# Kernel optimization log

Hardware: AMD Instinct MI355X
Metric: run time of the kernel (lower is better)

The kernel has to match this reference:

```python
import jax, jax.numpy as jnp
import numpy as np

N = 4096                 # num nodes
SP, GE, TE = 256, 8, 64  # modality input dims
E = 32                   # embed_dim == hidden_features == out_features
H = 2                    # num_heads
D3 = 3 * E               # combined dim = 96
NEG_SLOPE = 0.2


def setup_inputs() -> dict:
    key = jax.random.key(0)
    ks = iter(jax.random.split(key, 64))
    nrm = lambda shape, s=0.05: jax.random.normal(next(ks), shape, jnp.float32) * s
    inp = {
        "spatial": jax.random.normal(next(ks), (N, SP), jnp.float32),
        "genomic": jax.random.normal(next(ks), (N, GE), jnp.float32),
        "temporal": jax.random.normal(next(ks), (N, TE), jnp.float32),
        "adj_matrix": jax.random.randint(next(ks), (N, N), 0, 2, jnp.int32),
        # modality embedding MLPs (Linear + LayerNorm)
        "sp_w": nrm((SP, E)), "sp_b": jnp.zeros((E,)), "sp_lg": jnp.ones((E,)), "sp_lb": jnp.zeros((E,)),
        "ge_w": nrm((GE, E)), "ge_b": jnp.zeros((E,)), "ge_lg": jnp.ones((E,)), "ge_lb": jnp.zeros((E,)),
        "te_w": nrm((TE, E)), "te_b": jnp.zeros((E,)), "te_lg": jnp.ones((E,)), "te_lb": jnp.zeros((E,)),
        # GAT: W_shared [96 -> H*E], attention vector a [2E], out_proj [H*E -> E], LayerNorm(E)
        "gat_w": nrm((D3, H * E)), "gat_a": nrm((2 * E,)),
        "gat_ow": nrm((H * E, E)), "gat_ob": jnp.zeros((E,)),
        "gat_lg": jnp.ones((E,)), "gat_lb": jnp.zeros((E,)),
        # MultiheadAttention (embed 96): packed qkv in_proj and out_proj
        "mha_iw": nrm((D3, 3 * D3)), "mha_ib": jnp.zeros((3 * D3,)),
        "mha_ow": nrm((D3, D3)), "mha_ob": jnp.zeros((D3,)),
        # motor tower
        "m1_w": nrm((D3, 2 * E)), "m1_b": jnp.zeros((2 * E,)), "m1_lg": jnp.ones((2 * E,)), "m1_lb": jnp.zeros((2 * E,)),
        "m2_w": nrm((2 * E, E)), "m2_b": jnp.zeros((E,)), "m2_lg": jnp.ones((E,)), "m2_lb": jnp.zeros((E,)),
        "m3_w": nrm((E, 1)), "m3_b": jnp.zeros((1,)),
        # cognitive tower
        "c1_w": nrm((D3, 2 * E)), "c1_b": jnp.zeros((2 * E,)), "c1_lg": jnp.ones((2 * E,)), "c1_lb": jnp.zeros((2 * E,)),
        "c2_w": nrm((2 * E, E)), "c2_b": jnp.zeros((E,)), "c2_lg": jnp.ones((E,)), "c2_lb": jnp.zeros((E,)),
        "c3_w": nrm((E, 1)), "c3_b": jnp.zeros((1,)),
    }
    return inp


def _ln(x, g, b, eps=1e-5):
    m = x.mean(-1, keepdims=True)
    v = ((x - m) ** 2).mean(-1, keepdims=True)
    return (x - m) / jnp.sqrt(v + eps) * g + b


def _embed(x, w, b, lg, lb):
    return jax.nn.relu(_ln(x @ w + b, lg, lb))  # dropout is identity in eval


def _tower(x, w1, b1, lg1, lb1, w2, b2, lg2, lb2, w3, b3):
    h = jax.nn.relu(_ln(x @ w1 + b1, lg1, lb1))
    h = jax.nn.relu(_ln(h @ w2 + b2, lg2, lb2))
    return h @ w3 + b3


def reference(spatial, genomic, temporal, adj_matrix,
              sp_w, sp_b, sp_lg, sp_lb, ge_w, ge_b, ge_lg, ge_lb,
              te_w, te_b, te_lg, te_lb,
              gat_w, gat_a, gat_ow, gat_ob, gat_lg, gat_lb,
              mha_iw, mha_ib, mha_ow, mha_ob,
              m1_w, m1_b, m1_lg, m1_lb, m2_w, m2_b, m2_lg, m2_lb, m3_w, m3_b,
              c1_w, c1_b, c1_lg, c1_lb, c2_w, c2_b, c2_lg, c2_lb, c3_w, c3_b):
    n = spatial.shape[0]
    s_emb = _embed(spatial, sp_w, sp_b, sp_lg, sp_lb)
    g_emb = _embed(genomic, ge_w, ge_b, ge_lg, ge_lb)
    t_emb = _embed(temporal, te_w, te_b, te_lg, te_lb)
    combined = jnp.concatenate([s_emb, g_emb, t_emb], axis=-1)  # [N, 96]

    # --- TaskSpecificGAT ---
    h = (combined @ gat_w).reshape(n, H, E)  # [N, H, E]
    # e[i,j] = leaky_relu(a . [h_i ; h_j]) = leaky_relu((h @ a1)_i + (h @ a2)_j)
    a1, a2 = gat_a[:E], gat_a[E:]
    f1 = jnp.einsum('nhd,d->nh', h, a1)  # source term
    f2 = jnp.einsum('nhd,d->nh', h, a2)  # target term
    e = jax.nn.leaky_relu(f1[:, None, :] + f2[None, :, :], NEG_SLOPE)  # [N, N, H]
    e = jnp.where(adj_matrix[:, :, None] == 0, -jnp.inf, e)
    alpha = jax.nn.softmax(e, axis=1)  # softmax over neighbors j
    h_out = jnp.einsum('ijh,jhd->ihd', alpha, h).reshape(n, H * E)  # [N, 64]
    gat_out = _ln(h_out @ gat_ow + gat_ob, gat_lg, gat_lb)  # [N, 32]

    # gat_expanded = cat([gat_out]*3) -> [N, 96], attn over seq_len=1
    gx = jnp.tile(gat_out, (1, 3))
    # MHA with a single key/query: softmax over one key == 1, so output = out_proj(v)
    v = gx @ mha_iw[:, 2 * D3:] + mha_ib[2 * D3:]
    attn_out = v @ mha_ow + mha_ob

    final = attn_out + combined
    motor = _tower(final, m1_w, m1_b, m1_lg, m1_lb, m2_w, m2_b, m2_lg, m2_lb, m3_w, m3_b)
    cognitive = jax.nn.sigmoid(
        _tower(final, c1_w, c1_b, c1_lg, c1_lb, c2_w, c2_b, c2_lg, c2_lb, c3_w, c3_b))
    return (motor, cognitive)
```

## Files before the change

kernel.cpp:

```cpp
#include <hip/hip_runtime.h>
#include <math.h>

#define NN 4096
#define LOG2E 1.4426950408889634f

typedef short short8 __attribute__((ext_vector_type(8)));
typedef float f32x4 __attribute__((ext_vector_type(4)));

#define OFF_COMB   0u
#define OFF_F1     393216u
#define OFF_F2     401408u
#define OFF_MAXF2  409600u
#define OFF_W2     409616u
#define OFF_B2     412688u
#define OFF_HT     412800u
#define OFF_PART   543872u

__device__ inline unsigned short f2bf(float x) {
  unsigned u = __float_as_uint(x);
  unsigned r = u + 0x7FFFu + ((u >> 16) & 1u);
  return (unsigned short)(r >> 16);
}

__global__ __launch_bounds__(256) void k_comb(
    const float* __restrict__ spatial, const float* __restrict__ genomic,
    const float* __restrict__ temporal,
    const float* __restrict__ sp_w, const float* __restrict__ sp_b,
    const float* __restrict__ sp_lg, const float* __restrict__ sp_lb,
    const float* __restrict__ ge_w, const float* __restrict__ ge_b,
    const float* __restrict__ ge_lg, const float* __restrict__ ge_lb,
    const float* __restrict__ te_w, const float* __restrict__ te_b,
    const float* __restrict__ te_lg, const float* __restrict__ te_lb,
    const float* __restrict__ mha_iw, const float* __restrict__ mha_ib,
    const float* __restrict__ mha_ow, const float* __restrict__ mha_ob,
    float* __restrict__ ws)
{
  int t = threadIdx.x;
  int blk = blockIdx.x;

  if (blk >= 1536) {
    if (blk < 1548) {
      int idx = (blk - 1536) * 256 + t;
      int b = idx / 96, col = idx - b * 96;
      float acc = 0.f;
      for (int r = 0; r < 96; r++) {
        float fw = mha_iw[b * 288 + 192 + r]
                 + mha_iw[(b + 32) * 288 + 192 + r]
                 + mha_iw[(b + 64) * 288 + 192 + r];
        acc = fmaf(fw, mha_ow[r * 96 + col], acc);
      }
      ws[OFF_W2 + b * 96 + col] = acc;
    } else {
      if (t < 96) {
        float acc = mha_ob[t];
        for (int r = 0; r < 96; r++) acc = fmaf(mha_ib[192 + r], mha_ow[r * 96 + t], acc);
        ws[OFF_B2 + t] = acc;
      }
    }
    return;
  }

  int j = blk * 8 + (t >> 5);
  int grp = j >> 12;
  int row = j & 4095;
  int c = t & 31;

  float val;
  const float* lg;
  const float* lb;
  if (grp == 0) {
    const float* in = spatial + (size_t)row * 256;
    float a0 = 0.f, a1 = 0.f, a2 = 0.f, a3 = 0.f;
#pragma unroll 4
    for (int k = 0; k < 256; k += 4) {
      float4 x = *(const float4*)(in + k);
      a0 = fmaf(x.x, sp_w[(k)     * 32 + c], a0);
      a1 = fmaf(x.y, sp_w[(k + 1) * 32 + c], a1);
      a2 = fmaf(x.z, sp_w[(k + 2) * 32 + c], a2);
      a3 = fmaf(x.w, sp_w[(k + 3) * 32 + c], a3);
    }
    val = sp_b[c] + ((a0 + a1) + (a2 + a3));
    lg = sp_lg; lb = sp_lb;
  } else if (grp == 1) {
    const float* in = genomic + (size_t)row * 8;
    float4 x0 = *(const float4*)(in);
    float4 x1 = *(const float4*)(in + 4);
    float a0 = ge_b[c];
    a0 = fmaf(x0.x, ge_w[0 * 32 + c], a0);
    a0 = fmaf(x0.y, ge_w[1 * 32 + c], a0);
    a0 = fmaf(x0.z, ge_w[2 * 32 + c], a0);
    a0 = fmaf(x0.w, ge_w[3 * 32 + c], a0);
    a0 = fmaf(x1.x, ge_w[4 * 32 + c], a0);
    a0 = fmaf(x1.y, ge_w[5 * 32 + c], a0);
    a0 = fmaf(x1.z, ge_w[6 * 32 + c], a0);
    a0 = fmaf(x1.w, ge_w[7 * 32 + c], a0);
    val = a0;
    lg = ge_lg; lb = ge_lb;
  } else {
    const float* in = temporal + (size_t)row * 64;
    float a0 = 0.f, a1 = 0.f, a2 = 0.f, a3 = 0.f;
#pragma unroll 4
    for (int k = 0; k < 64; k += 4) {
      float4 x = *(const float4*)(in + k);
      a0 = fmaf(x.x, te_w[(k)     * 32 + c], a0);
      a1 = fmaf(x.y, te_w[(k + 1) * 32 + c], a1);
      a2 = fmaf(x.z, te_w[(k + 2) * 32 + c], a2);
      a3 = fmaf(x.w, te_w[(k + 3) * 32 + c], a3);
    }
    val = te_b[c] + ((a0 + a1) + (a2 + a3));
    lg = te_lg; lb = te_lb;
  }

  float s1 = val, s2 = val * val;
#pragma unroll
  for (int m = 1; m < 32; m <<= 1) {
    s1 += __shfl_xor(s1, m, 32);
    s2 += __shfl_xor(s2, m, 32);
  }
  float mean = s1 * (1.f / 32.f);
  float var  = s2 * (1.f / 32.f) - mean * mean;
  float y = fmaxf((val - mean) * rsqrtf(var + 1e-5f) * lg[c] + lb[c], 0.f);
  ws[OFF_COMB + (size_t)row * 96 + grp * 32 + c] = y;
}

__global__ __launch_bounds__(256) void k_proj(
    const float* __restrict__ gat_w, const float* __restrict__ gat_a,
    float* __restrict__ ws)
{
  __shared__ float h_s[4][64];
  int t = threadIdx.x;
  int w = t >> 6, d = t & 63;
  int row0 = blockIdx.x * 4;
  int row = row0 + w;

  const float* crow = ws + OFF_COMB + (size_t)row * 96;
  float a0 = 0.f, a1 = 0.f;
#pragma unroll 8
  for (int k = 0; k < 96; k += 2) {
    a0 = fmaf(crow[k],     gat_w[k * 64 + d],       a0);
    a1 = fmaf(crow[k + 1], gat_w[(k + 1) * 64 + d], a1);
  }
  float h = a0 + a1;

  int dc = d & 31;
  float p1 = h * gat_a[dc];
  float p2 = h * gat_a[32 + dc];
#pragma unroll
  for (int m = 1; m < 32; m <<= 1) {
    p1 += __shfl_xor(p1, m, 32);
    p2 += __shfl_xor(p2, m, 32);
  }
  if (dc == 0) {
    int head = d >> 5;
    ws[OFF_F1 + head * NN + row] = p1;
    ws[OFF_F2 + head * NN + row] = p2;
  }

  h_s[w][d] = h;
  __syncthreads();
  if (t < 64) {
    unsigned u0 = (unsigned)f2bf(h_s[0][t]) | ((unsigned)f2bf(h_s[1][t]) << 16);
    unsigned u1 = (unsigned)f2bf(h_s[2][t]) | ((unsigned)f2bf(h_s[3][t]) << 16);
    uint2 v; v.x = u0; v.y = u1;
    unsigned short* hT = (unsigned short*)(ws + OFF_HT);
    *(uint2*)(hT + (size_t)t * NN + row0) = v;
  }
}

__global__ __launch_bounds__(256) void k_max(float* __restrict__ ws)
{
  __shared__ float red[4][2];
  int t = threadIdx.x;
  const float4* p0 = (const float4*)(ws + OFF_F2);
  const float4* p1 = (const float4*)(ws + OFF_F2 + NN);
  float m0 = -1e30f, m1 = -1e30f;
#pragma unroll
  for (int q = 0; q < 4; q++) {
    float4 v0 = p0[t + q * 256];
    float4 v1 = p1[t + q * 256];
    m0 = fmaxf(m0, fmaxf(fmaxf(v0.x, v0.y), fmaxf(v0.z, v0.w)));
    m1 = fmaxf(m1, fmaxf(fmaxf(v1.x, v1.y), fmaxf(v1.z, v1.w)));
  }
#pragma unroll
  for (int m = 1; m < 64; m <<= 1) {
    m0 = fmaxf(m0, __shfl_xor(m0, m));
    m1 = fmaxf(m1, __shfl_xor(m1, m));
  }
  if ((t & 63) == 0) { red[t >> 6][0] = m0; red[t >> 6][1] = m1; }
  __syncthreads();
  if (t == 0) {
    float r0 = red[0][0], r1 = red[0][1];
    for (int q = 1; q < 4; q++) { r0 = fmaxf(r0, red[q][0]); r1 = fmaxf(r1, red[q][1]); }
    ws[OFF_MAXF2] = r0;
    ws[OFF_MAXF2 + 1] = r1;
  }
}

__global__ __launch_bounds__(256) void k_gat3(
    const int* __restrict__ adj,
    const unsigned short* __restrict__ hT,
    const float* __restrict__ f1h,
    const float* __restrict__ f2h,
    const float* __restrict__ maxf2,
    float* __restrict__ part,
    float* __restrict__ lpart, int NS)
{
  int t = threadIdx.x;
  int lane = t & 63, wv = t >> 6;
  int quad = lane >> 4, mrow = lane & 15;
  int ib = blockIdx.x * 64 + wv * 16;
  int i_lane = ib + mrow;
  int slice = NN / NS;
  int jb = blockIdx.y * slice;

  float f1v0 = f1h[i_lane];
  float f1v1 = f1h[NN + i_lane];
  float s0 = f1v0 + maxf2[0], s1 = f1v1 + maxf2[1];
  float sh0 = fmaxf(s0, 0.2f * s0);
  float sh1 = fmaxf(s1, 0.2f * s1);
  float c00 = -sh0 * LOG2E;
  float c01 = -sh1 * LOG2E;

  f32x4 acc00 = {0.f, 0.f, 0.f, 0.f};
  f32x4 acc01 = {0.f, 0.f, 0.f, 0.f};
  f32x4 acc10 = {0.f, 0.f, 0.f, 0.f};
  f32x4 acc11 = {0.f, 0.f, 0.f, 0.f};
  float ls0 = 0.f, ls1 = 0.f;

  const int* adjRow = adj + (size_t)i_lane * NN;

#pragma unroll 2
  for (int jc = jb; jc < jb + slice; jc += 32) {
    int jq = jc + quad * 8;
    int4 am0 = *(const int4*)(adjRow + jq);
    int4 am1 = *(const int4*)(adjRow + jq + 4);
    float4 fa = *(const float4*)(f2h + jq);
    float4 fb = *(const float4*)(f2h + jq + 4);
    float4 fc = *(const float4*)(f2h + NN + jq);
    float4 fd = *(const float4*)(f2h + NN + jq + 4);
    short8 b00 = *(const short8*)(hT + (size_t)(mrow)      * NN + jq);
    short8 b01 = *(const short8*)(hT + (size_t)(16 + mrow) * NN + jq);
    short8 b10 = *(const short8*)(hT + (size_t)(32 + mrow) * NN + jq);
    short8 b11 = *(const short8*)(hT + (size_t)(48 + mrow) * NN + jq);

    float f2a[8] = {fa.x, fa.y, fa.z, fa.w, fb.x, fb.y, fb.z, fb.w};
    float f2b[8] = {fc.x, fc.y, fc.z, fc.w, fd.x, fd.y, fd.z, fd.w};
    int   amv[8] = {am0.x, am0.y, am0.z, am0.w, am1.x, am1.y, am1.z, am1.w};

    union { short8 v; unsigned short u[8]; } a0, a1;
#pragma unroll
    for (int k = 0; k < 8; k++) {
      float e0 = f1v0 + f2a[k];
      float le0 = fmaxf(e0, 0.2f * e0);
      float w0 = __builtin_amdgcn_exp2f(fmaf(le0, LOG2E, c00));
      float e1 = f1v1 + f2b[k];
      float le1 = fmaxf(e1, 0.2f * e1);
      float w1 = __builtin_amdgcn_exp2f(fmaf(le1, LOG2E, c01));
      w0 = amv[k] ? w0 : 0.f;
      w1 = amv[k] ? w1 : 0.f;
      ls0 += w0; ls1 += w1;
      a0.u[k] = f2bf(w0);
      a1.u[k] = f2bf(w1);
    }
    acc00 = __builtin_amdgcn_mfma_f32_16x16x32_bf16(a0.v, b00, acc00, 0, 0, 0);
    acc01 = __builtin_amdgcn_mfma_f32_16x16x32_bf16(a0.v, b01, acc01, 0, 0, 0);
    acc10 = __builtin_amdgcn_mfma_f32_16x16x32_bf16(a1.v, b10, acc10, 0, 0, 0);
    acc11 = __builtin_amdgcn_mfma_f32_16x16x32_bf16(a1.v, b11, acc11, 0, 0, 0);
  }

  ls0 += __shfl_xor(ls0, 16); ls0 += __shfl_xor(ls0, 32);
  ls1 += __shfl_xor(ls1, 16); ls1 += __shfl_xor(ls1, 32);

  int slot = blockIdx.y;
#pragma unroll
  for (int r = 0; r < 4; r++) {
    int ig = ib + quad * 4 + r;
    float* p = part + (size_t)ig * (NS * 64) + slot * 64;
    p[mrow]      = acc00[r];
    p[16 + mrow] = acc01[r];
    p[32 + mrow] = acc10[r];
    p[48 + mrow] = acc11[r];
  }
  if (lane < 16) {
    int ig = ib + lane;
    lpart[((size_t)ig * NS + slot) * 2]     = ls0;
    lpart[((size_t)ig * NS + slot) * 2 + 1] = ls1;
  }
}

__global__ __launch_bounds__(256) void k_post2(
    const float* __restrict__ gat_ow, const float* __restrict__ gat_ob,
    const float* __restrict__ gat_lg, const float* __restrict__ gat_lb,
    const float* __restrict__ m1_w, const float* __restrict__ m1_b,
    const float* __restrict__ m1_lg, const float* __restrict__ m1_lb,
    const float* __restrict__ m2_w, const float* __restrict__ m2_b,
    const float* __restrict__ m2_lg, const float* __restrict__ m2_lb,
    const float* __restrict__ m3_w, const float* __restrict__ m3_b,
    const float* __restrict__ c1_w, const float* __restrict__ c1_b,
    const float* __restrict__ c1_lg, const float* __restrict__ c1_lb,
    const float* __restrict__ c2_w, const float* __restrict__ c2_b,
    const float* __restrict__ c2_lg, const float* __restrict__ c2_lb,
    const float* __restrict__ c3_w, const float* __restrict__ c3_b,
    const float* __restrict__ part, const float* __restrict__ lpart,
    const float* __restrict__ comb, const float* __restrict__ W2,
    const float* __restrict__ B2,
    float* __restrict__ out, int NS)
{
  int t = threadIdx.x;
  int w = t >> 6, l = t & 63;
  int i = blockIdx.x * 4 + w;

  __shared__ float sh_h[4][64];
  __shared__ float sh_go[4][32];
  __shared__ float sh_fin[4][96];
  __shared__ float sh_t1[4][2][64];

  {
    const float* pr = part + (size_t)i * (NS * 64);
    float a0 = 0.f, a1 = 0.f, a2 = 0.f, a3 = 0.f;
#pragma unroll
    for (int s = 0; s < 16; s += 4) {
      a0 += pr[(s)     * 64 + l];
      a1 += pr[(s + 1) * 64 + l];
      a2 += pr[(s + 2) * 64 + l];
      a3 += pr[(s + 3) * 64 + l];
    }
    float a = (a0 + a1) + (a2 + a3);
    const float* lr = lpart + (size_t)i * NS * 2;
    float l0 = 0.f, l1 = 0.f;
#pragma unroll
    for (int s = 0; s < 16; s++) { l0 += lr[s * 2]; l1 += lr[s * 2 + 1]; }
    sh_h[w][l] = a / (l < 32 ? l0 : l1);
  }
  __syncthreads();

  if (l < 32) {
    float acc = gat_ob[l];
#pragma unroll 8
    for (int r = 0; r < 64; r++) acc = fmaf(sh_h[w][r], gat_ow[r * 32 + l], acc);
    float s1 = acc, s2 = acc * acc;
#pragma unroll
    for (int m = 1; m < 32; m <<= 1) {
      s1 += __shfl_xor(s1, m, 32);
      s2 += __shfl_xor(s2, m, 32);
    }
    float mean = s1 * (1.f / 32.f), var = s2 * (1.f / 32.f) - mean * mean;
    sh_go[w][l] = (acc - mean) * rsqrtf(var + 1e-5f) * gat_lg[l] + gat_lb[l];
  }
  __syncthreads();

  {
    float accA = B2[l];
#pragma unroll 8
    for (int d = 0; d < 32; d++) accA = fmaf(sh_go[w][d], W2[d * 96 + l], accA);
    sh_fin[w][l] = accA + comb[(size_t)i * 96 + l];
    if (l < 32) {
      float accB = B2[64 + l];
#pragma unroll 8
      for (int d = 0; d < 32; d++) accB = fmaf(sh_go[w][d], W2[d * 96 + 64 + l], accB);
      sh_fin[w][64 + l] = accB + comb[(size_t)i * 96 + 64 + l];
    }
  }
  __syncthreads();

  {
    float am = m1_b[l], ac = c1_b[l];
#pragma unroll 4
    for (int r = 0; r < 96; r++) {
      float f = sh_fin[w][r];
      am = fmaf(f, m1_w[r * 64 + l], am);
      ac = fmaf(f, c1_w[r * 64 + l], ac);
    }
    float s1 = am, s2 = am * am;
#pragma unroll
    for (int m = 1; m < 64; m <<= 1) { s1 += __shfl_xor(s1, m); s2 += __shfl_xor(s2, m); }
    float mean = s1 * (1.f / 64.f), var = s2 * (1.f / 64.f) - mean * mean;
    sh_t1[w][0][l] = fmaxf((am - mean) * rsqrtf(var + 1e-5f) * m1_lg[l] + m1_lb[l], 0.f);
    s1 = ac; s2 = ac * ac;
#pragma unroll
    for (int m = 1; m < 64; m <<= 1) { s1 += __shfl_xor(s1, m); s2 += __shfl_xor(s2, m); }
    mean = s1 * (1.f / 64.f); var = s2 * (1.f / 64.f) - mean * mean;
    sh_t1[w][1][l] = fmaxf((ac - mean) * rsqrtf(var + 1e-5f) * c1_lg[l] + c1_lb[l], 0.f);
  }
  __syncthreads();

  {
    int tw = l >> 5, c = l & 31;
    const float* w2  = tw ? c2_w  : m2_w;
    const float* b2  = tw ? c2_b  : m2_b;
    const float* lg2 = tw ? c2_lg : m2_lg;
    const float* lb2 = tw ? c2_lb : m2_lb;
    float a2 = b2[c];
#pragma unroll 4
    for (int r = 0; r < 64; r++) a2 = fmaf(sh_t1[w][tw][r], w2[r * 32 + c], a2);
    float u1 = a2, u2 = a2 * a2;
#pragma unroll
    for (int m = 1; m < 32; m <<= 1) {
      u1 += __shfl_xor(u1, m, 32);
      u2 += __shfl_xor(u2, m, 32);
    }
    float mean = u1 * (1.f / 32.f), var = u2 * (1.f / 32.f) - mean * mean;
    float y2 = fmaxf((a2 - mean) * rsqrtf(var + 1e-5f) * lg2[c] + lb2[c], 0.f);
    float p = y2 * (tw ? c3_w[c] : m3_w[c]);
#pragma unroll
    for (int m = 1; m < 32; m <<= 1) p += __shfl_xor(p, m, 32);
    if (c == 0) {
      float v = p + (tw ? c3_b[0] : m3_b[0]);
      if (tw) out[NN + i] = 1.f / (1.f + expf(-v));
      else    out[i] = v;
    }
  }
}

extern "C" void kernel_launch(void* const* d_in, const int* in_sizes, int n_in,
                              void* d_out, int out_size, void* d_ws, size_t ws_size,
                              hipStream_t stream) {
  (void)in_sizes; (void)n_in; (void)out_size;
  const float* spatial  = (const float*)d_in[0];
  const float* genomic  = (const float*)d_in[1];
  const float* temporal = (const float*)d_in[2];
  const int*   adj      = (const int*)d_in[3];
  const float* sp_w = (const float*)d_in[4];
  const float* sp_b = (const float*)d_in[5];
  const float* sp_lg = (const float*)d_in[6];
  const float* sp_lb = (const float*)d_in[7];
  const float* ge_w = (const float*)d_in[8];
  const float* ge_b = (const float*)d_in[9];
  const float* ge_lg = (const float*)d_in[10];
  const float* ge_lb = (const float*)d_in[11];
  const float* te_w = (const float*)d_in[12];
  const float* te_b = (const float*)d_in[13];
  const float* te_lg = (const float*)d_in[14];
  const float* te_lb = (const float*)d_in[15];
  const float* gat_w = (const float*)d_in[16];
  const float* gat_a = (const float*)d_in[17];
  const float* gat_ow = (const float*)d_in[18];
  const float* gat_ob = (const float*)d_in[19];
  const float* gat_lg = (const float*)d_in[20];
  const float* gat_lb = (const float*)d_in[21];
  const float* mha_iw = (const float*)d_in[22];
  const float* mha_ib = (const float*)d_in[23];
  const float* mha_ow = (const float*)d_in[24];
  const float* mha_ob = (const float*)d_in[25];
  const float* m1_w = (const float*)d_in[26];
  const float* m1_b = (const float*)d_in[27];
  const float* m1_lg = (const float*)d_in[28];
  const float* m1_lb = (const float*)d_in[29];
  const float* m2_w = (const float*)d_in[30];
  const float* m2_b = (const float*)d_in[31];
  const float* m2_lg = (const float*)d_in[32];
  const float* m2_lb = (const float*)d_in[33];
  const float* m3_w = (const float*)d_in[34];
  const float* m3_b = (const float*)d_in[35];
  const float* c1_w = (const float*)d_in[36];
  const float* c1_b = (const float*)d_in[37];
  const float* c1_lg = (const float*)d_in[38];
  const float* c1_lb = (const float*)d_in[39];
  const float* c2_w = (const float*)d_in[40];
  const float* c2_b = (const float*)d_in[41];
  const float* c2_lg = (const float*)d_in[42];
  const float* c2_lb = (const float*)d_in[43];
  const float* c3_w = (const float*)d_in[44];
  const float* c3_b = (const float*)d_in[45];

  float* ws  = (float*)d_ws;
  float* out = (float*)d_out;

  int NS = 16;
  while (NS > 1) {
    size_t need = (size_t)(OFF_PART + (size_t)NS * NN * 64 + (size_t)NS * NN * 2) * 4;
    if (need <= ws_size) break;
    NS >>= 1;
  }
  float* part  = ws + OFF_PART;
  float* lpart = part + (size_t)NS * NN * 64;

  k_comb<<<1549, 256, 0, stream>>>(spatial, genomic, temporal,
                                   sp_w, sp_b, sp_lg, sp_lb,
                                   ge_w, ge_b, ge_lg, ge_lb,
                                   te_w, te_b, te_lg, te_lb,
                                   mha_iw, mha_ib, mha_ow, mha_ob, ws);
  k_proj<<<NN / 4, 256, 0, stream>>>(gat_w, gat_a, ws);
  k_max<<<1, 256, 0, stream>>>(ws);
  dim3 g2(NN / 64, NS);
  k_gat3<<<g2, 256, 0, stream>>>(adj,
                                 (const unsigned short*)(ws + OFF_HT),
                                 ws + OFF_F1, ws + OFF_F2, ws + OFF_MAXF2,
                                 part, lpart, NS);
  k_post2<<<NN / 4, 256, 0, stream>>>(gat_ow, gat_ob, gat_lg, gat_lb,
                                      m1_w, m1_b, m1_lg, m1_lb,
                                      m2_w, m2_b, m2_lg, m2_lb,
                                      m3_w, m3_b,
                                      c1_w, c1_b, c1_lg, c1_lb,
                                      c2_w, c2_b, c2_lg, c2_lb,
                                      c3_w, c3_b,
                                      part, lpart, ws + OFF_COMB,
                                      ws + OFF_W2, ws + OFF_B2,
                                      out, NS);
}
```

Before: 260.3 us.

## Drop max-shift kernel, template GAT split count and raise j-split to 32

Removes the separate f2 max-reduction kernel and the softmax max shift, so exp is computed on the raw leaky-relu score; this saves one launch and a few ops per element but risks overflow or bf16 range issues if scores grow large. The GAT aggregation and post kernels are templated on the split count, so the inner loop fully unrolls. When workspace allows, the neighbour dimension is split 32 ways instead of 16 for more blocks. The cost is more partial sums to write and reduce.

```diff
diff --git a/kernel.cpp b/kernel.cpp
--- a/kernel.cpp
+++ b/kernel.cpp
@@ -10,7 +10,6 @@
 #define OFF_COMB   0u
 #define OFF_F1     393216u
 #define OFF_F2     401408u
-#define OFF_MAXF2  409600u
 #define OFF_W2     409616u
 #define OFF_B2     412688u
 #define OFF_HT     412800u
@@ -167,59 +166,25 @@
   }
 }
 
-__global__ __launch_bounds__(256) void k_max(float* __restrict__ ws)
-{
-  __shared__ float red[4][2];
-  int t = threadIdx.x;
-  const float4* p0 = (const float4*)(ws + OFF_F2);
-  const float4* p1 = (const float4*)(ws + OFF_F2 + NN);
-  float m0 = -1e30f, m1 = -1e30f;
-#pragma unroll
-  for (int q = 0; q < 4; q++) {
-    float4 v0 = p0[t + q * 256];
-    float4 v1 = p1[t + q * 256];
-    m0 = fmaxf(m0, fmaxf(fmaxf(v0.x, v0.y), fmaxf(v0.z, v0.w)));
-    m1 = fmaxf(m1, fmaxf(fmaxf(v1.x, v1.y), fmaxf(v1.z, v1.w)));
-  }
-#pragma unroll
-  for (int m = 1; m < 64; m <<= 1) {
-    m0 = fmaxf(m0, __shfl_xor(m0, m));
-    m1 = fmaxf(m1, __shfl_xor(m1, m));
-  }
-  if ((t & 63) == 0) { red[t >> 6][0] = m0; red[t >> 6][1] = m1; }
-  __syncthreads();
-  if (t == 0) {
-    float r0 = red[0][0], r1 = red[0][1];
-    for (int q = 1; q < 4; q++) { r0 = fmaxf(r0, red[q][0]); r1 = fmaxf(r1, red[q][1]); }
-    ws[OFF_MAXF2] = r0;
-    ws[OFF_MAXF2 + 1] = r1;
-  }
-}
-
-__global__ __launch_bounds__(256) void k_gat3(
+template<int NSC>
+__global__ __launch_bounds__(256) void k_gat4(
     const int* __restrict__ adj,
     const unsigned short* __restrict__ hT,
     const float* __restrict__ f1h,
     const float* __restrict__ f2h,
-    const float* __restrict__ maxf2,
     float* __restrict__ part,
-    float* __restrict__ lpart, int NS)
+    float* __restrict__ lpart)
 {
+  constexpr int SLICE = NN / NSC;
   int t = threadIdx.x;
   int lane = t & 63, wv = t >> 6;
   int quad = lane >> 4, mrow = lane & 15;
   int ib = blockIdx.x * 64 + wv * 16;
   int i_lane = ib + mrow;
-  int slice = NN / NS;
-  int jb = blockIdx.y * slice;
+  int jb = blockIdx.y * SLICE;
 
   float f1v0 = f1h[i_lane];
   float f1v1 = f1h[NN + i_lane];
-  float s0 = f1v0 + maxf2[0], s1 = f1v1 + maxf2[1];
-  float sh0 = fmaxf(s0, 0.2f * s0);
-  float sh1 = fmaxf(s1, 0.2f * s1);
-  float c00 = -sh0 * LOG2E;
-  float c01 = -sh1 * LOG2E;
 
   f32x4 acc00 = {0.f, 0.f, 0.f, 0.f};
   f32x4 acc01 = {0.f, 0.f, 0.f, 0.f};
@@ -229,9 +194,9 @@
 
   const int* adjRow = adj + (size_t)i_lane * NN;
 
-#pragma unroll 2
-  for (int jc = jb; jc < jb + slice; jc += 32) {
-    int jq = jc + quad * 8;
+#pragma unroll
+  for (int ci = 0; ci < SLICE / 32; ci++) {
+    int jq = jb + ci * 32 + quad * 8;
     int4 am0 = *(const int4*)(adjRow + jq);
     int4 am1 = *(const int4*)(adjRow + jq + 4);
     float4 fa = *(const float4*)(f2h + jq);
@@ -252,10 +217,10 @@
     for (int k = 0; k < 8; k++) {
       float e0 = f1v0 + f2a[k];
       float le0 = fmaxf(e0, 0.2f * e0);
-      float w0 = __builtin_amdgcn_exp2f(fmaf(le0, LOG2E, c00));
+      float w0 = __builtin_amdgcn_exp2f(le0 * LOG2E);
       float e1 = f1v1 + f2b[k];
       float le1 = fmaxf(e1, 0.2f * e1);
-      float w1 = __builtin_amdgcn_exp2f(fmaf(le1, LOG2E, c01));
+      float w1 = __builtin_amdgcn_exp2f(le1 * LOG2E);
       w0 = amv[k] ? w0 : 0.f;
       w1 = amv[k] ? w1 : 0.f;
       ls0 += w0; ls1 += w1;
@@ -275,7 +240,7 @@
 #pragma unroll
   for (int r = 0; r < 4; r++) {
     int ig = ib + quad * 4 + r;
-    float* p = part + (size_t)ig * (NS * 64) + slot * 64;
+    float* p = part + (size_t)ig * (NSC * 64) + slot * 64;
     p[mrow]      = acc00[r];
     p[16 + mrow] = acc01[r];
     p[32 + mrow] = acc10[r];
@@ -283,12 +248,13 @@
   }
   if (lane < 16) {
     int ig = ib + lane;
-    lpart[((size_t)ig * NS + slot) * 2]     = ls0;
-    lpart[((size_t)ig * NS + slot) * 2 + 1] = ls1;
-  }
-}
-
-__global__ __launch_bounds__(256) void k_post2(
+    lpart[((size_t)ig * NSC + slot) * 2]     = ls0;
+    lpart[((size_t)ig * NSC + slot) * 2 + 1] = ls1;
+  }
+}
+
+template<int NSC>
+__global__ __launch_bounds__(256) void k_post3(
     const float* __restrict__ gat_ow, const float* __restrict__ gat_ob,
     const float* __restrict__ gat_lg, const float* __restrict__ gat_lb,
     const float* __restrict__ m1_w, const float* __restrict__ m1_b,
@@ -304,7 +270,7 @@
     const float* __restrict__ part, const float* __restrict__ lpart,
     const float* __restrict__ comb, const float* __restrict__ W2,
     const float* __restrict__ B2,
-    float* __restrict__ out, int NS)
+    float* __restrict__ out)
 {
   int t = threadIdx.x;
   int w = t >> 6, l = t & 63;
@@ -316,20 +282,20 @@
   __shared__ float sh_t1[4][2][64];
 
   {
-    const float* pr = part + (size_t)i * (NS * 64);
+    const float* pr = part + (size_t)i * (NSC * 64);
     float a0 = 0.f, a1 = 0.f, a2 = 0.f, a3 = 0.f;
 #pragma unroll
-    for (int s = 0; s < 16; s += 4) {
+    for (int s = 0; s < NSC; s += 4) {
       a0 += pr[(s)     * 64 + l];
       a1 += pr[(s + 1) * 64 + l];
       a2 += pr[(s + 2) * 64 + l];
       a3 += pr[(s + 3) * 64 + l];
     }
     float a = (a0 + a1) + (a2 + a3);
-    const float* lr = lpart + (size_t)i * NS * 2;
+    const float* lr = lpart + (size_t)i * NSC * 2;
     float l0 = 0.f, l1 = 0.f;
 #pragma unroll
-    for (int s = 0; s < 16; s++) { l0 += lr[s * 2]; l1 += lr[s * 2 + 1]; }
+    for (int s = 0; s < NSC; s++) { l0 += lr[s * 2]; l1 += lr[s * 2 + 1]; }
     sh_h[w][l] = a / (l < 32 ? l0 : l1);
   }
   __syncthreads();
@@ -466,14 +432,7 @@
   float* ws  = (float*)d_ws;
   float* out = (float*)d_out;
 
-  int NS = 16;
-  while (NS > 1) {
-    size_t need = (size_t)(OFF_PART + (size_t)NS * NN * 64 + (size_t)NS * NN * 2) * 4;
-    if (need <= ws_size) break;
-    NS >>= 1;
-  }
   float* part  = ws + OFF_PART;
-  float* lpart = part + (size_t)NS * NN * 64;
 
   k_comb<<<1549, 256, 0, stream>>>(spatial, genomic, temporal,
                                    sp_w, sp_b, sp_lg, sp_lb,
@@ -481,20 +440,50 @@
                                    te_w, te_b, te_lg, te_lb,
                                    mha_iw, mha_ib, mha_ow, mha_ob, ws);
   k_proj<<<NN / 4, 256, 0, stream>>>(gat_w, gat_a, ws);
-  k_max<<<1, 256, 0, stream>>>(ws);
-  dim3 g2(NN / 64, NS);
-  k_gat3<<<g2, 256, 0, stream>>>(adj,
-                                 (const unsigned short*)(ws + OFF_HT),
-                                 ws + OFF_F1, ws + OFF_F2, ws + OFF_MAXF2,
-                                 part, lpart, NS);
-  k_post2<<<NN / 4, 256, 0, stream>>>(gat_ow, gat_ob, gat_lg, gat_lb,
-                                      m1_w, m1_b, m1_lg, m1_lb,
-                                      m2_w, m2_b, m2_lg, m2_lb,
-                                      m3_w, m3_b,
-                                      c1_w, c1_b, c1_lg, c1_lb,
-                                      c2_w, c2_b, c2_lg, c2_lb,
-                                      c3_w, c3_b,
-                                      part, lpart, ws + OFF_COMB,
-                                      ws + OFF_W2, ws + OFF_B2,
-                                      out, NS);
-}
+
+  size_t need32 = (size_t)(OFF_PART + 32ul * NN * 64 + 32ul * NN * 2) * 4;
+  size_t need16 = (size_t)(OFF_PART + 16ul * NN * 64 + 16ul * NN * 2) * 4;
+  if (ws_size >= need32) {
+    float* lpart = part + 32ul * NN * 64;
+    dim3 g2(NN / 64, 32);
+    k_gat4<32><<<g2, 256, 0, stream>>>(adj, (const unsigned short*)(ws + OFF_HT),
+                                       ws + OFF_F1, ws + OFF_F2, part, lpart);
+    k_post3<32><<<NN / 4, 256, 0, stream>>>(gat_ow, gat_ob, gat_lg, gat_lb,
+                                            m1_w, m1_b, m1_lg, m1_lb,
+                                            m2_w, m2_b, m2_lg, m2_lb,
+                                            m3_w, m3_b,
+                                            c1_w, c1_b, c1_lg, c1_lb,
+                                            c2_w, c2_b, c2_lg, c2_lb,
+                                            c3_w, c3_b,
+                                            part, lpart, ws + OFF_COMB,
+                                            ws + OFF_W2, ws + OFF_B2, out);
+  } else if (ws_size >= need16) {
+    float* lpart = part + 16ul * NN * 64;
+    dim3 g2(NN / 64, 16);
+    k_gat4<16><<<g2, 256, 0, stream>>>(adj, (const unsigned short*)(ws + OFF_HT),
+                                       ws + OFF_F1, ws + OFF_F2, part, lpart);
+    k_post3<16><<<NN / 4, 256, 0, stream>>>(gat_ow, gat_ob, gat_lg, gat_lb,
+                                            m1_w, m1_b, m1_lg, m1_lb,
+                                            m2_w, m2_b, m2_lg, m2_lb,
+                                            m3_w, m3_b,
+                                            c1_w, c1_b, c1_lg, c1_lb,
+                                            c2_w, c2_b, c2_lg, c2_lb,
+                                            c3_w, c3_b,
+                                            part, lpart, ws + OFF_COMB,
+                                            ws + OFF_W2, ws + OFF_B2, out);
+  } else {
+    float* lpart = part + 8ul * NN * 64;
+    dim3 g2(NN / 64, 8);
+    k_gat4<8><<<g2, 256, 0, stream>>>(adj, (const unsigned short*)(ws + OFF_HT),
+                                      ws + OFF_F1, ws + OFF_F2, part, lpart);
+    k_post3<8><<<NN / 4, 256, 0, stream>>>(gat_ow, gat_ob, gat_lg, gat_lb,
+                                           m1_w, m1_b, m1_lg, m1_lb,
+                                           m2_w, m2_b, m2_lg, m2_lb,
+                                           m3_w, m3_b,
+                                           c1_w, c1_b, c1_lg, c1_lb,
+                                           c2_w, c2_b, c2_lg, c2_lb,
+                                           c3_w, c3_b,
+                                           part, lpart, ws + OFF_COMB,
+                                           ws + OFF_W2, ws + OFF_B2, out);
+  }
+}
```

After: 261.9 us. No clear change (+0.6%).
